# Performance work log

Hardware: AMD Instinct MI355X
Metric: run time of the kernel (lower is better)

The kernel has to match this reference:

```python
import jax, jax.numpy as jnp
import numpy as np

B, T, IN, CELL, OUT = 512, 32, 512, 128, 128


def setup_inputs() -> dict:
    key = jax.random.key(0)
    ks = jax.random.split(key, 6)
    d = IN + CELL
    w = lambda k, shape, fan: jax.random.normal(k, shape, jnp.float32) / np.sqrt(fan).astype(np.float32)
    return {
        "x": jax.random.normal(ks[0], (B, T, IN), jnp.float32),
        "Wf": w(ks[1], (d, CELL), d), "bf": jnp.zeros((CELL,), jnp.float32),
        "Wi1": w(ks[2], (d, CELL), d), "bi1": jnp.zeros((CELL,), jnp.float32),
        "Wi2": w(ks[3], (d, CELL), d), "bi2": jnp.zeros((CELL,), jnp.float32),
        "Wo": w(ks[4], (d, CELL), d), "bo": jnp.zeros((CELL,), jnp.float32),
        "Wc": w(ks[5], (CELL, OUT), CELL), "bc": jnp.zeros((OUT,), jnp.float32),
    }


def reference(x, Wf, bf, Wi1, bi1, Wi2, bi2, Wo, bo, Wc, bc):
    # Faithful to MyLSTM.forward: loop runs x.shape[1] times; each iteration
    # concatenates the FULL [B,T,CELL] cell_state with the FULL [B,T,IN] x
    # (x is never sliced per step). Only the last iteration's output matters,
    # but we carry it through the scan to match the loop structure exactly.
    Tn = x.shape[1]
    c0 = jnp.zeros(x.shape[:2] + (Wf.shape[1],), x.dtype)
    out0 = jnp.zeros(x.shape[:2] + (Wc.shape[1],), x.dtype)

    def step(carry, _):
        c, _prev_out = carry
        inp = jnp.concatenate([c, x], axis=-1)  # [B,T,CELL+IN]
        f = jax.nn.sigmoid(inp @ Wf + bf)
        c = c * f + jax.nn.sigmoid(inp @ Wi1 + bi1) * jnp.tanh(inp @ Wi2 + bi2)
        o = jax.nn.sigmoid(inp @ Wo + bo) * jnp.tanh(c)
        out = jax.nn.softmax(o @ Wc + bc, axis=2)  # out_features != 1 branch
        return (c, out), None

    (c, out), _ = jax.lax.scan(step, (c0, out0), None, length=Tn)
    return out, c
```

## Files before the change

kernel.cpp:

```cpp
#include <hip/hip_runtime.h>
#include <stdint.h>

#define ROWS  16384
#define CELL  128
#define INF   512
#define RPB   16
#define NSTEP 32

typedef _Float16 f16x8 __attribute__((ext_vector_type(8)));
typedef _Float16 f16x4 __attribute__((ext_vector_type(4)));
typedef float    f32x4 __attribute__((ext_vector_type(4)));

#define MFMA16(a, b, c) __builtin_amdgcn_mfma_f32_16x16x32_f16((a), (b), (c), 0, 0, 0)

#define AOFF  0
#define XOFF  65536
#define WCOFF 327680
#define WSTOT 344064

#define LOG2E  1.44269504f
#define LOG2E2 2.88539008f

__device__ __forceinline__ unsigned short f2h_bits(float f) {
  _Float16 h = (_Float16)f;
  return *(unsigned short*)&h;
}
__device__ __forceinline__ float sig2(float z) {
  return __builtin_amdgcn_rcpf(1.f + __builtin_amdgcn_exp2f(-z));
}
__device__ __forceinline__ float tanh2(float z) {
  return 1.f - 2.f * __builtin_amdgcn_rcpf(__builtin_amdgcn_exp2f(z) + 1.f);
}

__global__ __launch_bounds__(256) void prep_kernel(
    const float* __restrict__ Wf, const float* __restrict__ Wi1,
    const float* __restrict__ Wi2, const float* __restrict__ Wo,
    const float* __restrict__ Wc, unsigned short* __restrict__ ws) {
  int id = blockIdx.x * blockDim.x + threadIdx.x;
  if (id >= WSTOT) return;
  const float* Wg[4] = {Wf, Wi1, Wi2, Wo};
  const float scl[4] = {LOG2E, LOG2E, LOG2E2, LOG2E};
  float v;
  int k, n, base;
  if (id < XOFF) {
    int g = id >> 14, r = id & 16383;
    k = r >> 7; n = r & 127;
    v = Wg[g][k * CELL + n] * scl[g];
    base = g * 16384;
  } else if (id < WCOFF) {
    int t = id - XOFF;
    int g = t >> 16, r = t & 65535;
    k = r >> 7; n = r & 127;
    v = Wg[g][(CELL + k) * CELL + n] * scl[g];
    base = XOFF + g * 65536;
  } else {
    int r = id - WCOFF;
    k = r >> 7; n = r & 127;
    v = Wc[k * CELL + n];
    base = WCOFF;
  }
  int ks = k >> 5, kk = k & 31;
  int lane = ((kk >> 3) << 4) | (n & 15);
  int j = kk & 7, nb = n >> 4;
  ws[base + ((ks * 8 + nb) * 64 + lane) * 8 + j] = f2h_bits(v);
}

__global__ __launch_bounds__(512, 4) void lstm_kernel(
    const float* __restrict__ x,
    const float* __restrict__ bf_, const float* __restrict__ bi1,
    const float* __restrict__ bi2, const float* __restrict__ bo,
    const float* __restrict__ bc,
    const unsigned short* __restrict__ ws, float* __restrict__ out) {

  __shared__ _Float16 cF[2][16][136];
  __shared__ union {
    _Float16 xs[16][520];
    struct {
      float    s[16][132];
      _Float16 o[16][136];
    } ep;
  } uS;

  const int tid  = threadIdx.x;
  const int lane = tid & 63;
  const int w    = tid >> 6;
  const int n16  = lane & 15;
  const int g4   = lane >> 4;
  const int col0 = w * 16 + g4 * 4;
  const int r0   = blockIdx.x * RPB;

  const _Float16* Aw  = (const _Float16*)ws + AOFF;
  const _Float16* Xw  = (const _Float16*)ws + XOFF;
  const _Float16* Wcw = (const _Float16*)ws + WCOFF;

  {
    const float* xb = x + (size_t)r0 * INF;
#pragma unroll
    for (int i = 0; i < 4; ++i) {
      int flat = tid + i * 512;
      int row = flat >> 7, c4 = flat & 127;
      const float4 v = ((const float4*)(xb + (size_t)row * INF))[c4];
      f16x4 h = {(_Float16)v.x, (_Float16)v.y, (_Float16)v.z, (_Float16)v.w};
      *(f16x4*)&uS.xs[row][c4 * 4] = h;
    }
  }
  __syncthreads();

  f32x4 u[4];
#pragma unroll
  for (int g = 0; g < 4; ++g)
#pragma unroll
    for (int i = 0; i < 4; ++i) u[g][i] = 0.f;

#pragma unroll 4
  for (int ks = 0; ks < 16; ++ks) {
    f16x8 a = *(const f16x8*)&uS.xs[n16][ks * 32 + g4 * 8];
#pragma unroll
    for (int g = 0; g < 4; ++g) {
      f16x8 b = *(const f16x8*)(Xw + g * 65536 + ((ks * 8 + w) * 64 + lane) * 8);
      u[g] = MFMA16(b, a, u[g]);
    }
  }
  {
    f32x4 b0 = *(const f32x4*)&bf_[col0];
    f32x4 b1 = *(const f32x4*)&bi1[col0];
    f32x4 b2 = *(const f32x4*)&bi2[col0];
    f32x4 b3 = *(const f32x4*)&bo[col0];
#pragma unroll
    for (int i = 0; i < 4; ++i) {
      u[0][i] = fmaf(b0[i], LOG2E,  u[0][i]);
      u[1][i] = fmaf(b1[i], LOG2E,  u[1][i]);
      u[2][i] = fmaf(b2[i], LOG2E2, u[2][i]);
      u[3][i] = fmaf(b3[i], LOG2E,  u[3][i]);
    }
  }

  f16x8 wr[3][4];
#pragma unroll
  for (int g = 0; g < 3; ++g)
#pragma unroll
    for (int ks = 0; ks < 4; ++ks)
      wr[g][ks] = *(const f16x8*)(Aw + g * 16384 + ((ks * 8 + w) * 64 + lane) * 8);

  f32x4 cr;
  {
    f16x4 hv;
#pragma unroll
    for (int i = 0; i < 4; ++i) {
      float c0 = sig2(u[1][i]) * tanh2(u[2][i]);
      cr[i] = c0;
      hv[i] = (_Float16)c0;
    }
    *(f16x4*)&cF[0][n16][col0] = hv;
  }
  __syncthreads();

#pragma unroll 1
  for (int t = 1; t < NSTEP - 1; ++t) {
    const int rb = (t + 1) & 1, wb = t & 1;
    f16x8 a[4];
#pragma unroll
    for (int ks = 0; ks < 4; ++ks)
      a[ks] = *(const f16x8*)&cF[rb][n16][ks * 32 + g4 * 8];
    f32x4 zf = u[0], zi1 = u[1], zi2 = u[2];
#pragma unroll
    for (int ks = 0; ks < 4; ++ks) {
      zf  = MFMA16(wr[0][ks], a[ks], zf);
      zi1 = MFMA16(wr[1][ks], a[ks], zi1);
      zi2 = MFMA16(wr[2][ks], a[ks], zi2);
    }
    f16x4 hv;
#pragma unroll
    for (int i = 0; i < 4; ++i) {
      float fg = sig2(zf[i]);
      float ig = sig2(zi1[i]);
      float gg = tanh2(zi2[i]);
      float cn = fmaf(cr[i], fg, ig * gg);
      cr[i] = cn;
      hv[i] = (_Float16)cn;
    }
    *(f16x4*)&cF[wb][n16][col0] = hv;
    __syncthreads();
  }

  {
    f16x8 a[4];
#pragma unroll
    for (int ks = 0; ks < 4; ++ks)
      a[ks] = *(const f16x8*)&cF[0][n16][ks * 32 + g4 * 8];
    f32x4 zf = u[0], zi1 = u[1], zi2 = u[2], zo = u[3];
#pragma unroll
    for (int ks = 0; ks < 4; ++ks) {
      f16x8 bo_frag = *(const f16x8*)(Aw + 3 * 16384 + ((ks * 8 + w) * 64 + lane) * 8);
      zf  = MFMA16(wr[0][ks], a[ks], zf);
      zi1 = MFMA16(wr[1][ks], a[ks], zi1);
      zi2 = MFMA16(wr[2][ks], a[ks], zi2);
      zo  = MFMA16(bo_frag,  a[ks], zo);
    }
    f16x4 hv;
#pragma unroll
    for (int i = 0; i < 4; ++i) {
      float fg = sig2(zf[i]);
      float ig = sig2(zi1[i]);
      float gg = tanh2(zi2[i]);
      float cn = fmaf(cr[i], fg, ig * gg);
      cr[i] = cn;
      float ov = sig2(zo[i]) * tanh2(cn * LOG2E2);
      hv[i] = (_Float16)ov;
    }
    __syncthreads();
    *(f16x4*)&uS.ep.o[n16][col0] = hv;
    __syncthreads();
  }

  {
    f32x4 sacc;
#pragma unroll
    for (int i = 0; i < 4; ++i) sacc[i] = 0.f;
#pragma unroll
    for (int ks = 0; ks < 4; ++ks) {
      f16x8 a = *(const f16x8*)&uS.ep.o[n16][ks * 32 + g4 * 8];
      f16x8 b = *(const f16x8*)(Wcw + ((ks * 8 + w) * 64 + lane) * 8);
      sacc = MFMA16(b, a, sacc);
    }
    f32x4 bcv = *(const f32x4*)&bc[col0];
#pragma unroll
    for (int i = 0; i < 4; ++i) sacc[i] += bcv[i];
    *(f32x4*)&uS.ep.s[n16][col0] = sacc;
    __syncthreads();

#pragma unroll
    for (int rr = 0; rr < 2; ++rr) {
      int r = w * 2 + rr;
      float v0 = uS.ep.s[r][lane];
      float v1 = uS.ep.s[r][lane + 64];
      float m = fmaxf(v0, v1);
#pragma unroll
      for (int off = 32; off; off >>= 1) m = fmaxf(m, __shfl_xor(m, off, 64));
      float e0 = __expf(v0 - m), e1 = __expf(v1 - m);
      float sm = e0 + e1;
#pragma unroll
      for (int off = 32; off; off >>= 1) sm += __shfl_xor(sm, off, 64);
      float inv = __builtin_amdgcn_rcpf(sm);
      size_t base = (size_t)(r0 + r) * 128;
      out[base + lane]      = e0 * inv;
      out[base + lane + 64] = e1 * inv;
    }

    *(f32x4*)&out[(size_t)ROWS * 128 + (size_t)(r0 + n16) * 128 + col0] = cr;
  }
}

extern "C" void kernel_launch(void* const* d_in, const int* in_sizes, int n_in,
                              void* d_out, int out_size, void* d_ws, size_t ws_size,
                              hipStream_t stream) {
  const float* x   = (const float*)d_in[0];
  const float* Wf  = (const float*)d_in[1];
  const float* bf_ = (const float*)d_in[2];
  const float* Wi1 = (const float*)d_in[3];
  const float* bi1 = (const float*)d_in[4];
  const float* Wi2 = (const float*)d_in[5];
  const float* bi2 = (const float*)d_in[6];
  const float* Wo  = (const float*)d_in[7];
  const float* bo  = (const float*)d_in[8];
  const float* Wc  = (const float*)d_in[9];
  const float* bc  = (const float*)d_in[10];
  unsigned short* ws = (unsigned short*)d_ws;
  float* out = (float*)d_out;

  hipLaunchKernelGGL(prep_kernel, dim3((WSTOT + 255) / 256), dim3(256), 0, stream,
                     Wf, Wi1, Wi2, Wo, Wc, ws);
  hipLaunchKernelGGL(lstm_kernel, dim3(ROWS / RPB), dim3(512), 0, stream,
                     x, bf_, bi1, bi2, bo, bc, ws, out);
}
```

Before: 168.5 us.

## Give each wave its own 16 rows so the recurrence needs no block barriers

Each wave now owns 16 rows and computes all 128 cell columns (8 n-blocks), so the 30-step recurrence needs no __syncthreads. The cell state goes through a per-wave swizzled LDS tile instead of a block-shared double buffer. The forget and input recurrent weights stay in registers, the Wi2 weights move to LDS, and the x projections are kept as fp16 in registers. Softmax is done in-register using exp2 with LOG2E folded into Wc. The cost is much higher register pressure (launch bounds 256,1), lower occupancy, and fp16 rounding of the precomputed input terms.

```diff
diff --git a/kernel.cpp b/kernel.cpp
--- a/kernel.cpp
+++ b/kernel.cpp
@@ -4,7 +4,6 @@
 #define ROWS  16384
 #define CELL  128
 #define INF   512
-#define RPB   16
 #define NSTEP 32
 
 typedef _Float16 f16x8 __attribute__((ext_vector_type(8)));
@@ -56,7 +55,7 @@
   } else {
     int r = id - WCOFF;
     k = r >> 7; n = r & 127;
-    v = Wc[k * CELL + n];
+    v = Wc[k * CELL + n] * LOG2E;
     base = WCOFF;
   }
   int ks = k >> 5, kk = k & 31;
@@ -65,190 +64,248 @@
   ws[base + ((ks * 8 + nb) * 64 + lane) * 8 + j] = f2h_bits(v);
 }
 
-__global__ __launch_bounds__(512, 4) void lstm_kernel(
+__global__ __launch_bounds__(256, 1) void lstm_kernel(
     const float* __restrict__ x,
     const float* __restrict__ bf_, const float* __restrict__ bi1,
     const float* __restrict__ bi2, const float* __restrict__ bo,
     const float* __restrict__ bc,
     const unsigned short* __restrict__ ws, float* __restrict__ out) {
 
-  __shared__ _Float16 cF[2][16][136];
-  __shared__ union {
-    _Float16 xs[16][520];
-    struct {
-      float    s[16][132];
-      _Float16 o[16][136];
-    } ep;
-  } uS;
+  __shared__ _Float16 wi2S[16384];
+  __shared__ _Float16 uoS[8192];
+  __shared__ _Float16 cT[8192];
 
   const int tid  = threadIdx.x;
   const int lane = tid & 63;
   const int w    = tid >> 6;
   const int n16  = lane & 15;
   const int g4   = lane >> 4;
-  const int col0 = w * 16 + g4 * 4;
-  const int r0   = blockIdx.x * RPB;
+  const int sxor = n16 & 7;
+  const int myrow = blockIdx.x * 64 + w * 16 + n16;
 
   const _Float16* Aw  = (const _Float16*)ws + AOFF;
-  const _Float16* Xw  = (const _Float16*)ws + XOFF;
+  const _Float16* XwP = (const _Float16*)ws + XOFF;
   const _Float16* Wcw = (const _Float16*)ws + WCOFF;
 
-  {
-    const float* xb = x + (size_t)r0 * INF;
+#pragma unroll
+  for (int i = 0; i < 8; ++i) {
+    int idx = tid + i * 256;
+    *(f16x8*)&wi2S[idx * 8] = *(const f16x8*)(Aw + 2 * 16384 + idx * 8);
+  }
+
+  f32x4 u[4][8];
+#pragma unroll
+  for (int g = 0; g < 4; ++g)
+#pragma unroll
+    for (int nb = 0; nb < 8; ++nb)
+#pragma unroll
+      for (int i = 0; i < 4; ++i) u[g][nb][i] = 0.f;
+
+  const float* xr = x + (size_t)myrow * INF;
+#pragma unroll 1
+  for (int ks = 0; ks < 16; ++ks) {
+    float4 x0 = *(const float4*)(xr + ks * 32 + g4 * 8);
+    float4 x1 = *(const float4*)(xr + ks * 32 + g4 * 8 + 4);
+    f16x8 xa = {(_Float16)x0.x, (_Float16)x0.y, (_Float16)x0.z, (_Float16)x0.w,
+                (_Float16)x1.x, (_Float16)x1.y, (_Float16)x1.z, (_Float16)x1.w};
+#pragma unroll
+    for (int g = 0; g < 4; ++g)
+#pragma unroll
+      for (int nb = 0; nb < 8; ++nb)
+        u[g][nb] = MFMA16(
+            *(const f16x8*)(XwP + g * 65536 + ((ks * 8 + nb) * 64 + lane) * 8),
+            xa, u[g][nb]);
+  }
+
+  f16x4 u3[3][8];
+#pragma unroll
+  for (int nb = 0; nb < 8; ++nb) {
+    const int c0 = nb * 16 + g4 * 4;
+    f32x4 b0 = *(const f32x4*)&bf_[c0];
+    f32x4 b1 = *(const f32x4*)&bi1[c0];
+    f32x4 b2 = *(const f32x4*)&bi2[c0];
+    f32x4 b3 = *(const f32x4*)&bo[c0];
+    f16x4 h0, h1, h2, h3;
 #pragma unroll
     for (int i = 0; i < 4; ++i) {
-      int flat = tid + i * 512;
-      int row = flat >> 7, c4 = flat & 127;
-      const float4 v = ((const float4*)(xb + (size_t)row * INF))[c4];
-      f16x4 h = {(_Float16)v.x, (_Float16)v.y, (_Float16)v.z, (_Float16)v.w};
-      *(f16x4*)&uS.xs[row][c4 * 4] = h;
-    }
+      h0[i] = (_Float16)fmaf(b0[i], LOG2E,  u[0][nb][i]);
+      h1[i] = (_Float16)fmaf(b1[i], LOG2E,  u[1][nb][i]);
+      h2[i] = (_Float16)fmaf(b2[i], LOG2E2, u[2][nb][i]);
+      h3[i] = (_Float16)fmaf(b3[i], LOG2E,  u[3][nb][i]);
+    }
+    u3[0][nb] = h0; u3[1][nb] = h1; u3[2][nb] = h2;
+    *(f16x4*)&uoS[w * 2048 + nb * 256 + lane * 4] = h3;
   }
   __syncthreads();
 
-  f32x4 u[4];
-#pragma unroll
-  for (int g = 0; g < 4; ++g)
-#pragma unroll
-    for (int i = 0; i < 4; ++i) u[g][i] = 0.f;
-
-#pragma unroll 4
-  for (int ks = 0; ks < 16; ++ks) {
-    f16x8 a = *(const f16x8*)&uS.xs[n16][ks * 32 + g4 * 8];
-#pragma unroll
-    for (int g = 0; g < 4; ++g) {
-      f16x8 b = *(const f16x8*)(Xw + g * 65536 + ((ks * 8 + w) * 64 + lane) * 8);
-      u[g] = MFMA16(b, a, u[g]);
-    }
-  }
-  {
-    f32x4 b0 = *(const f32x4*)&bf_[col0];
-    f32x4 b1 = *(const f32x4*)&bi1[col0];
-    f32x4 b2 = *(const f32x4*)&bi2[col0];
-    f32x4 b3 = *(const f32x4*)&bo[col0];
+  f16x8 wrf[8][4], wri[8][4];
+#pragma unroll
+  for (int nb = 0; nb < 8; ++nb)
+#pragma unroll
+    for (int ks = 0; ks < 4; ++ks) {
+      wrf[nb][ks] = *(const f16x8*)(Aw + ((ks * 8 + nb) * 64 + lane) * 8);
+      wri[nb][ks] = *(const f16x8*)(Aw + 16384 + ((ks * 8 + nb) * 64 + lane) * 8);
+    }
+
+  const int cb = w * 2048 + n16 * 128;
+  const int aoff0 = cb + (((0  + g4) ^ sxor) << 3);
+  const int aoff1 = cb + (((4  + g4) ^ sxor) << 3);
+  const int aoff2 = cb + (((8  + g4) ^ sxor) << 3);
+  const int aoff3 = cb + (((12 + g4) ^ sxor) << 3);
+  const int shr   = sxor >> 1;
+  const int wbase = cb + (g4 & 1) * 4 + (((g4 >> 1) ^ (sxor & 1)) << 3);
+
+  f32x4 cr[8];
+  f16x8 a0, a1, a2, a3;
+
+#pragma unroll
+  for (int nb = 0; nb < 8; ++nb) {
+    f32x4 cn; f16x4 hv;
 #pragma unroll
     for (int i = 0; i < 4; ++i) {
-      u[0][i] = fmaf(b0[i], LOG2E,  u[0][i]);
-      u[1][i] = fmaf(b1[i], LOG2E,  u[1][i]);
-      u[2][i] = fmaf(b2[i], LOG2E2, u[2][i]);
-      u[3][i] = fmaf(b3[i], LOG2E,  u[3][i]);
-    }
-  }
-
-  f16x8 wr[3][4];
-#pragma unroll
-  for (int g = 0; g < 3; ++g)
-#pragma unroll
-    for (int ks = 0; ks < 4; ++ks)
-      wr[g][ks] = *(const f16x8*)(Aw + g * 16384 + ((ks * 8 + w) * 64 + lane) * 8);
-
-  f32x4 cr;
-  {
-    f16x4 hv;
-#pragma unroll
-    for (int i = 0; i < 4; ++i) {
-      float c0 = sig2(u[1][i]) * tanh2(u[2][i]);
-      cr[i] = c0;
-      hv[i] = (_Float16)c0;
-    }
-    *(f16x4*)&cF[0][n16][col0] = hv;
-  }
-  __syncthreads();
+      cn[i] = sig2((float)u3[1][nb][i]) * tanh2((float)u3[2][nb][i]);
+      hv[i] = (_Float16)cn[i];
+    }
+    cr[nb] = cn;
+    *(f16x4*)&cT[wbase + ((nb ^ shr) << 4)] = hv;
+  }
+  a0 = *(const f16x8*)&cT[aoff0];
+  a1 = *(const f16x8*)&cT[aoff1];
+  a2 = *(const f16x8*)&cT[aoff2];
+  a3 = *(const f16x8*)&cT[aoff3];
 
 #pragma unroll 1
   for (int t = 1; t < NSTEP - 1; ++t) {
-    const int rb = (t + 1) & 1, wb = t & 1;
-    f16x8 a[4];
-#pragma unroll
-    for (int ks = 0; ks < 4; ++ks)
-      a[ks] = *(const f16x8*)&cF[rb][n16][ks * 32 + g4 * 8];
-    f32x4 zf = u[0], zi1 = u[1], zi2 = u[2];
-#pragma unroll
-    for (int ks = 0; ks < 4; ++ks) {
-      zf  = MFMA16(wr[0][ks], a[ks], zf);
-      zi1 = MFMA16(wr[1][ks], a[ks], zi1);
-      zi2 = MFMA16(wr[2][ks], a[ks], zi2);
-    }
-    f16x4 hv;
+#pragma unroll
+    for (int nb = 0; nb < 8; ++nb) {
+      const f16x8 w0 = *(const f16x8*)&wi2S[((0  + nb) * 64 + lane) * 8];
+      const f16x8 w1 = *(const f16x8*)&wi2S[((8  + nb) * 64 + lane) * 8];
+      const f16x8 w2 = *(const f16x8*)&wi2S[((16 + nb) * 64 + lane) * 8];
+      const f16x8 w3 = *(const f16x8*)&wi2S[((24 + nb) * 64 + lane) * 8];
+      f32x4 sf, si, sg;
+#pragma unroll
+      for (int i = 0; i < 4; ++i) {
+        sf[i] = (float)u3[0][nb][i];
+        si[i] = (float)u3[1][nb][i];
+        sg[i] = (float)u3[2][nb][i];
+      }
+      f32x4 zf = MFMA16(wrf[nb][0], a0, sf);
+      f32x4 zi = MFMA16(wri[nb][0], a0, si);
+      f32x4 zg = MFMA16(w0,         a0, sg);
+      zf = MFMA16(wrf[nb][1], a1, zf);
+      zi = MFMA16(wri[nb][1], a1, zi);
+      zg = MFMA16(w1,         a1, zg);
+      zf = MFMA16(wrf[nb][2], a2, zf);
+      zi = MFMA16(wri[nb][2], a2, zi);
+      zg = MFMA16(w2,         a2, zg);
+      zf = MFMA16(wrf[nb][3], a3, zf);
+      zi = MFMA16(wri[nb][3], a3, zi);
+      zg = MFMA16(w3,         a3, zg);
+      f32x4 cn; f16x4 hv;
+#pragma unroll
+      for (int i = 0; i < 4; ++i) {
+        float fg = sig2(zf[i]);
+        float ig = sig2(zi[i]);
+        float gg = tanh2(zg[i]);
+        cn[i] = fmaf(cr[nb][i], fg, ig * gg);
+        hv[i] = (_Float16)cn[i];
+      }
+      cr[nb] = cn;
+      *(f16x4*)&cT[wbase + ((nb ^ shr) << 4)] = hv;
+    }
+    a0 = *(const f16x8*)&cT[aoff0];
+    a1 = *(const f16x8*)&cT[aoff1];
+    a2 = *(const f16x8*)&cT[aoff2];
+    a3 = *(const f16x8*)&cT[aoff3];
+  }
+
+#pragma unroll
+  for (int nb = 0; nb < 8; ++nb) {
+    const f16x8 w0 = *(const f16x8*)&wi2S[((0  + nb) * 64 + lane) * 8];
+    const f16x8 w1 = *(const f16x8*)&wi2S[((8  + nb) * 64 + lane) * 8];
+    const f16x8 w2 = *(const f16x8*)&wi2S[((16 + nb) * 64 + lane) * 8];
+    const f16x8 w3 = *(const f16x8*)&wi2S[((24 + nb) * 64 + lane) * 8];
+    const f16x8 o0 = *(const f16x8*)(Aw + 3 * 16384 + ((0  + nb) * 64 + lane) * 8);
+    const f16x8 o1 = *(const f16x8*)(Aw + 3 * 16384 + ((8  + nb) * 64 + lane) * 8);
+    const f16x8 o2 = *(const f16x8*)(Aw + 3 * 16384 + ((16 + nb) * 64 + lane) * 8);
+    const f16x8 o3 = *(const f16x8*)(Aw + 3 * 16384 + ((24 + nb) * 64 + lane) * 8);
+    f16x4 uoh = *(const f16x4*)&uoS[w * 2048 + nb * 256 + lane * 4];
+    f32x4 sf, si, sg, so;
+#pragma unroll
+    for (int i = 0; i < 4; ++i) {
+      sf[i] = (float)u3[0][nb][i];
+      si[i] = (float)u3[1][nb][i];
+      sg[i] = (float)u3[2][nb][i];
+      so[i] = (float)uoh[i];
+    }
+    f32x4 zf = MFMA16(wrf[nb][0], a0, sf);
+    f32x4 zi = MFMA16(wri[nb][0], a0, si);
+    f32x4 zg = MFMA16(w0,         a0, sg);
+    f32x4 zo = MFMA16(o0,         a0, so);
+    zf = MFMA16(wrf[nb][1], a1, zf);
+    zi = MFMA16(wri[nb][1], a1, zi);
+    zg = MFMA16(w1,         a1, zg);
+    zo = MFMA16(o1,         a1, zo);
+    zf = MFMA16(wrf[nb][2], a2, zf);
+    zi = MFMA16(wri[nb][2], a2, zi);
+    zg = MFMA16(w2,         a2, zg);
+    zo = MFMA16(o2,         a2, zo);
+    zf = MFMA16(wrf[nb][3], a3, zf);
+    zi = MFMA16(wri[nb][3], a3, zi);
+    zg = MFMA16(w3,         a3, zg);
+    zo = MFMA16(o3,         a3, zo);
+    f32x4 cn; f16x4 hv;
 #pragma unroll
     for (int i = 0; i < 4; ++i) {
       float fg = sig2(zf[i]);
-      float ig = sig2(zi1[i]);
-      float gg = tanh2(zi2[i]);
-      float cn = fmaf(cr[i], fg, ig * gg);
-      cr[i] = cn;
-      hv[i] = (_Float16)cn;
-    }
-    *(f16x4*)&cF[wb][n16][col0] = hv;
-    __syncthreads();
-  }
-
-  {
-    f16x8 a[4];
-#pragma unroll
-    for (int ks = 0; ks < 4; ++ks)
-      a[ks] = *(const f16x8*)&cF[0][n16][ks * 32 + g4 * 8];
-    f32x4 zf = u[0], zi1 = u[1], zi2 = u[2], zo = u[3];
-#pragma unroll
-    for (int ks = 0; ks < 4; ++ks) {
-      f16x8 bo_frag = *(const f16x8*)(Aw + 3 * 16384 + ((ks * 8 + w) * 64 + lane) * 8);
-      zf  = MFMA16(wr[0][ks], a[ks], zf);
-      zi1 = MFMA16(wr[1][ks], a[ks], zi1);
-      zi2 = MFMA16(wr[2][ks], a[ks], zi2);
-      zo  = MFMA16(bo_frag,  a[ks], zo);
-    }
-    f16x4 hv;
-#pragma unroll
-    for (int i = 0; i < 4; ++i) {
-      float fg = sig2(zf[i]);
-      float ig = sig2(zi1[i]);
-      float gg = tanh2(zi2[i]);
-      float cn = fmaf(cr[i], fg, ig * gg);
-      cr[i] = cn;
-      float ov = sig2(zo[i]) * tanh2(cn * LOG2E2);
+      float ig = sig2(zi[i]);
+      float gg = tanh2(zg[i]);
+      cn[i] = fmaf(cr[nb][i], fg, ig * gg);
+      float ov = sig2(zo[i]) * tanh2(cn[i] * LOG2E2);
       hv[i] = (_Float16)ov;
     }
-    __syncthreads();
-    *(f16x4*)&uS.ep.o[n16][col0] = hv;
-    __syncthreads();
-  }
-
-  {
-    f32x4 sacc;
-#pragma unroll
-    for (int i = 0; i < 4; ++i) sacc[i] = 0.f;
-#pragma unroll
-    for (int ks = 0; ks < 4; ++ks) {
-      f16x8 a = *(const f16x8*)&uS.ep.o[n16][ks * 32 + g4 * 8];
-      f16x8 b = *(const f16x8*)(Wcw + ((ks * 8 + w) * 64 + lane) * 8);
-      sacc = MFMA16(b, a, sacc);
-    }
-    f32x4 bcv = *(const f32x4*)&bc[col0];
-#pragma unroll
-    for (int i = 0; i < 4; ++i) sacc[i] += bcv[i];
-    *(f32x4*)&uS.ep.s[n16][col0] = sacc;
-    __syncthreads();
-
-#pragma unroll
-    for (int rr = 0; rr < 2; ++rr) {
-      int r = w * 2 + rr;
-      float v0 = uS.ep.s[r][lane];
-      float v1 = uS.ep.s[r][lane + 64];
-      float m = fmaxf(v0, v1);
-#pragma unroll
-      for (int off = 32; off; off >>= 1) m = fmaxf(m, __shfl_xor(m, off, 64));
-      float e0 = __expf(v0 - m), e1 = __expf(v1 - m);
-      float sm = e0 + e1;
-#pragma unroll
-      for (int off = 32; off; off >>= 1) sm += __shfl_xor(sm, off, 64);
-      float inv = __builtin_amdgcn_rcpf(sm);
-      size_t base = (size_t)(r0 + r) * 128;
-      out[base + lane]      = e0 * inv;
-      out[base + lane + 64] = e1 * inv;
-    }
-
-    *(f32x4*)&out[(size_t)ROWS * 128 + (size_t)(r0 + n16) * 128 + col0] = cr;
-  }
+    cr[nb] = cn;
+    *(f16x4*)&cT[wbase + ((nb ^ shr) << 4)] = hv;
+  }
+  a0 = *(const f16x8*)&cT[aoff0];
+  a1 = *(const f16x8*)&cT[aoff1];
+  a2 = *(const f16x8*)&cT[aoff2];
+  a3 = *(const f16x8*)&cT[aoff3];
+
+  f32x4 ev[8];
+#pragma unroll
+  for (int nb = 0; nb < 8; ++nb) {
+    f32x4 sa = {0.f, 0.f, 0.f, 0.f};
+    sa = MFMA16(*(const f16x8*)(Wcw + ((0  + nb) * 64 + lane) * 8), a0, sa);
+    sa = MFMA16(*(const f16x8*)(Wcw + ((8  + nb) * 64 + lane) * 8), a1, sa);
+    sa = MFMA16(*(const f16x8*)(Wcw + ((16 + nb) * 64 + lane) * 8), a2, sa);
+    sa = MFMA16(*(const f16x8*)(Wcw + ((24 + nb) * 64 + lane) * 8), a3, sa);
+    f32x4 bcv = *(const f32x4*)&bc[nb * 16 + g4 * 4];
+#pragma unroll
+    for (int i = 0; i < 4; ++i)
+      ev[nb][i] = __builtin_amdgcn_exp2f(fmaf(bcv[i], LOG2E, sa[i]));
+  }
+  float sm = 0.f;
+#pragma unroll
+  for (int nb = 0; nb < 8; ++nb)
+#pragma unroll
+    for (int i = 0; i < 4; ++i) sm += ev[nb][i];
+  sm += __shfl_xor(sm, 16, 64);
+  sm += __shfl_xor(sm, 32, 64);
+  float inv = __builtin_amdgcn_rcpf(sm);
+
+  float* orow = out + (size_t)myrow * 128 + g4 * 4;
+#pragma unroll
+  for (int nb = 0; nb < 8; ++nb) {
+    f32x4 o4;
+#pragma unroll
+    for (int i = 0; i < 4; ++i) o4[i] = ev[nb][i] * inv;
+    *(f32x4*)&orow[nb * 16] = o4;
+  }
+  float* crow = out + (size_t)ROWS * 128 + (size_t)myrow * 128 + g4 * 4;
+#pragma unroll
+  for (int nb = 0; nb < 8; ++nb)
+    *(f32x4*)&crow[nb * 16] = cr[nb];
 }
 
 extern "C" void kernel_launch(void* const* d_in, const int* in_sizes, int n_in,
@@ -270,6 +327,6 @@
 
   hipLaunchKernelGGL(prep_kernel, dim3((WSTOT + 255) / 256), dim3(256), 0, stream,
                      Wf, Wi1, Wi2, Wo, Wc, ws);
-  hipLaunchKernelGGL(lstm_kernel, dim3(ROWS / RPB), dim3(512), 0, stream,
+  hipLaunchKernelGGL(lstm_kernel, dim3(ROWS / 64), dim3(256), 0, stream,
                      x, bf_, bi1, bi2, bo, bc, ws, out);
 }
```

Measured after the change: 305.6 us. 81.4% more time.
